# Kernel tuning notes

Measured on AMD Instinct MI355X. Metric: run time of the kernel, lower is better.

The kernel has to match this reference:

```python
import jax, jax.numpy as jnp
import numpy as np

N, E, R, B, IN, H, OUT, P = 20000, 320000, 8, 8, 128, 256, 128, 100000
LN_EPS = 1e-5


def _xavier(key, shape):
    fan_in, fan_out = shape[-2], shape[-1]
    lim = float(np.sqrt(6.0 / (fan_in + fan_out)))
    return jax.random.uniform(key, shape, jnp.float32, -lim, lim)


def setup_inputs() -> dict:
    key = jax.random.key(0)
    ks = iter(jax.random.split(key, 64))
    inp = {}
    inp['x'] = jax.random.normal(next(ks), (N, IN), jnp.float32)
    inp['edge_index'] = jax.random.randint(next(ks), (2, E), 0, N, jnp.int32)
    inp['edge_type'] = jax.random.randint(next(ks), (E,), 0, R, jnp.int32)
    inp['gene_pairs'] = jax.random.randint(next(ks), (2, P), 0, N, jnp.int32)
    dims = [(IN, H), (H, H), (H, H), (H, OUT)]  # per-layer (in_ch, out_ch)
    for i, (ic, oc) in enumerate(dims):
        inp[f'basis{i}'] = _xavier(next(ks), (B, ic, oc))
        inp[f'att{i}'] = _xavier(next(ks), (R, B))
        inp[f'root{i}'] = _xavier(next(ks), (ic, oc))
        inp[f'relatt{i}'] = jnp.ones((R,), jnp.float32)
        inp[f'g{i}'] = jnp.ones((oc,), jnp.float32)
        inp[f'b{i}'] = jnp.zeros((oc,), jnp.float32)
    inp['res0'] = _xavier(next(ks), (IN, H))   # in_ch != out_ch at layer 0
    inp['res3'] = _xavier(next(ks), (H, OUT))  # and at layer 3
    # decoder: 3*OUT -> H -> H//2 -> H//4 -> 1
    ddims = [(3 * OUT, H), (H, H // 2), (H // 2, H // 4), (H // 4, 1)]
    for i, (ic, oc) in enumerate(ddims):
        inp[f'dW{i}'] = _xavier(next(ks), (ic, oc))
        inp[f'db{i}'] = jnp.zeros((oc,), jnp.float32)
        if i < 3:
            inp[f'dg{i}'] = jnp.ones((oc,), jnp.float32)
            inp[f'dbb{i}'] = jnp.zeros((oc,), jnp.float32)
    return inp


def _ln(h, g, b):
    m = h.mean(-1, keepdims=True)
    v = ((h - m) ** 2).mean(-1, keepdims=True)
    return (h - m) * jax.lax.rsqrt(v + LN_EPS) * g + b


def _conv(x, src, dst, et, basis, att, root_w, rel_att):
    # W_r = sum_b att[r,b] * B_b ; message = a_{r(e)} * x_src @ W_{r(e)}
    # Since the message is linear, aggregate x_src per (dst, relation) first
    # (segment_sum), then apply the R small GEMMs once - same math, no [E,in,out].
    n, d = x.shape
    weight = jnp.einsum('rb,bio->rio', att, basis)          # [R,in,out]
    a = jax.nn.softmax(rel_att)                              # [R]
    seg = dst.astype(jnp.int32) * R + et.astype(jnp.int32)   # [(node,rel)] segment ids
    agg = jax.ops.segment_sum(x[src], seg, num_segments=n * R).reshape(n, R, d)
    out = jnp.einsum('nri,rio->no', agg, weight * a[:, None, None])
    return out + x @ root_w


def reference(x, edge_index, edge_type, gene_pairs,
              basis0, att0, root0, relatt0, g0, b0, res0,
              basis1, att1, root1, relatt1, g1, b1,
              basis2, att2, root2, relatt2, g2, b2,
              basis3, att3, root3, relatt3, g3, b3, res3,
              dW0, db0, dg0, dbb0, dW1, db1, dg1, dbb1,
              dW2, db2, dg2, dbb2, dW3, db3):
    src, dst = edge_index[0], edge_index[1]
    layers = [
        (basis0, att0, root0, relatt0, g0, b0, res0),
        (basis1, att1, root1, relatt1, g1, b1, None),
        (basis2, att2, root2, relatt2, g2, b2, None),
        (basis3, att3, root3, relatt3, g3, b3, res3),
    ]
    h = x
    for i, (bs, at, rt, ra, g, b, res) in enumerate(layers):
        h_in = h
        h = _conv(h, src, dst, edge_type, bs, at, rt, ra)
        h = _ln(h, g, b)
        h = h + (h_in @ res if res is not None else h_in)
        if i < len(layers) - 1:
            h = jax.nn.gelu(h, approximate=False)
    z = h  # [N, OUT]
    zi, zj = z[gene_pairs[0]], z[gene_pairs[1]]
    pe = jnp.concatenate([zi + zj, zi * zj, jnp.abs(zi - zj)], axis=-1)
    d = jax.nn.gelu(_ln(pe @ dW0 + db0, dg0, dbb0), approximate=False)
    d = jax.nn.gelu(_ln(d @ dW1 + db1, dg1, dbb1), approximate=False)
    d = jax.nn.gelu(_ln(d @ dW2 + db2, dg2, dbb2), approximate=False)
    logits = (d @ dW3 + db3).squeeze(-1)  # [P]
    return logits, z
```

## Files before the change

kernel.cpp:

```cpp
#include <hip/hip_runtime.h>
#include <hip/hip_bf16.h>
#include <math.h>
#include <cstddef>
#include <stdint.h>

#define NN 20000
#define EE 320000
#define RR 8
#define PP 100000
#define NR (NN * RR)

typedef __hip_bfloat16 bf16;
typedef __attribute__((ext_vector_type(8))) short short8;
typedef __attribute__((ext_vector_type(4))) short short4v;
typedef __attribute__((ext_vector_type(4))) float floatx4;
typedef __attribute__((ext_vector_type(4))) int intx4;

__device__ __forceinline__ float b2f(bf16 v) { return __bfloat162float(v); }
__device__ __forceinline__ bf16 f2b(float v) { return __float2bfloat16(v); }
__device__ __forceinline__ float bits2f(unsigned short u) {
  unsigned int i = ((unsigned int)u) << 16; float f; __builtin_memcpy(&f, &i, 4); return f;
}
__device__ __forceinline__ short f2bits(float f) {
  bf16 h = __float2bfloat16(f); short s; __builtin_memcpy(&s, &h, 2); return s;
}
__device__ __forceinline__ float gelu_f(float x) {
  float t = x * (0.7978845608f + 0.0356774081f * x * x);
  float s = exp2f(-2.885390082f * t);
  return x * __builtin_amdgcn_rcpf(1.f + s);
}
__device__ __forceinline__ void async_copy16(void* lds, const void* g) {
  __builtin_amdgcn_global_load_lds((const __attribute__((address_space(1))) void*)g,
                                   (__attribute__((address_space(3))) void*)lds, 16, 0, 0);
}
__device__ __forceinline__ const short8* frag_at(const bf16* base, int row, int q) {
  return (const short8*)(base + row * 64 + (((q) ^ (row & 7)) << 3));
}
__device__ __forceinline__ const short8* frag256(const bf16* base, int row, int col64, int q) {
  return (const short8*)(base + row * 256 + col64 + (((q) ^ (row & 7)) << 3));
}
__device__ __forceinline__ int idx128(int row, int qg) {
  return row * 128 + ((qg >> 3) << 6) + (((qg & 7) ^ (row & 7)) << 3);
}

__global__ void hist_k(const int* __restrict__ dst, const int* __restrict__ et,
                       int* __restrict__ counts) {
  int e = blockIdx.x * 256 + threadIdx.x;
  if (e >= EE) return;
  atomicAdd(&counts[dst[e] * RR + et[e]], 1);
}

__global__ void scan1_k(const int* __restrict__ counts, int* __restrict__ prefix,
                        int* __restrict__ bsums) {
  __shared__ int tmp[256];
  int i = blockIdx.x * 256 + threadIdx.x;
  int v = counts[i];
  tmp[threadIdx.x] = v; __syncthreads();
  for (int off = 1; off < 256; off <<= 1) {
    int x = (threadIdx.x >= off) ? tmp[threadIdx.x - off] : 0;
    __syncthreads();
    tmp[threadIdx.x] += x;
    __syncthreads();
  }
  prefix[i] = tmp[threadIdx.x] - v;
  if (threadIdx.x == 255) bsums[blockIdx.x] = tmp[255];
}

__global__ void scan2_k(int* __restrict__ bsums, int nb) {
  __shared__ int tmp[256];
  __shared__ int carry;
  if (threadIdx.x == 0) carry = 0;
  __syncthreads();
  for (int base = 0; base < nb; base += 256) {
    int i = base + threadIdx.x;
    int v = (i < nb) ? bsums[i] : 0;
    tmp[threadIdx.x] = v; __syncthreads();
    for (int off = 1; off < 256; off <<= 1) {
      int x = (threadIdx.x >= off) ? tmp[threadIdx.x - off] : 0;
      __syncthreads();
      tmp[threadIdx.x] += x;
      __syncthreads();
    }
    int c = carry;
    if (i < nb) bsums[i] = c + tmp[threadIdx.x] - v;
    __syncthreads();
    if (threadIdx.x == 255) carry = c + tmp[255];
    __syncthreads();
  }
}

__global__ void scan3_k(int* __restrict__ prefix, const int* __restrict__ bsums) {
  int i = blockIdx.x * 256 + threadIdx.x;
  prefix[i] += bsums[blockIdx.x];
}

__global__ void scatter_k(const int* __restrict__ src, const int* __restrict__ dst,
                          const int* __restrict__ et, const int* __restrict__ segstart,
                          int* __restrict__ cursor, int* __restrict__ ssrc) {
  int e = blockIdx.x * 256 + threadIdx.x;
  if (e >= EE) return;
  int s = dst[e] * RR + et[e];
  int pos = atomicAdd(&cursor[s], 1);
  ssrc[segstart[s] + pos] = src[e];
}

__global__ void cvt_bf16_k(const float* __restrict__ in, bf16* __restrict__ out, int n) {
  int i = blockIdx.x * 256 + threadIdx.x;
  if (i < n) out[i] = f2b(in[i]);
}

__global__ void softmax4_k(const float* r0, const float* r1, const float* r2,
                           const float* r3, float* __restrict__ a) {
  if (threadIdx.x == 0) {
    const float* rs[4] = {r0, r1, r2, r3};
    for (int l = 0; l < 4; ++l) {
      float mx = -1e30f;
      for (int i = 0; i < RR; ++i) mx = fmaxf(mx, rs[l][i]);
      float e[RR]; float s = 0.f;
      for (int i = 0; i < RR; ++i) { e[i] = expf(rs[l][i] - mx); s += e[i]; }
      for (int i = 0; i < RR; ++i) a[l * RR + i] = e[i] / s;
    }
  }
}

__global__ void transpose_k(const float* __restrict__ in, bf16* __restrict__ out,
                            int rows, int cols) {
  int idx = blockIdx.x * 256 + threadIdx.x;
  if (idx >= rows * cols) return;
  int r = idx / cols, c = idx - r * cols;
  out[(size_t)c * rows + r] = f2b(in[idx]);
}

__global__ void transpose_pe_k(const float* __restrict__ wb, const float* __restrict__ wc,
                               bf16* __restrict__ wpe) {
  int idx = blockIdx.x * 256 + threadIdx.x;
  if (idx >= 128 * 256) return;
  int k = idx >> 8;
  int o = idx & 255;
  wpe[(size_t)o * 256 + k] = f2b(wb[idx]);
  wpe[(size_t)o * 256 + 128 + k] = f2b(wc[idx]);
}

__global__ void prep_w_k(const float* __restrict__ basis, const float* __restrict__ att,
                         const float* __restrict__ root, const float* __restrict__ a,
                         bf16* __restrict__ Wt, int ic, int icsh, int oc, int ocsh) {
  int idx = blockIdx.x * 256 + threadIdx.x;
  int cols = 9 * ic;
  if (idx >= cols * oc) return;
  int o = idx & (oc - 1);
  int col = idx >> ocsh;
  int r = col >> icsh;
  int k = col & (ic - 1);
  float val;
  if (r < RR) {
    float acc = 0.f;
    for (int bb = 0; bb < RR; ++bb)
      acc += att[r * RR + bb] * basis[((size_t)bb * ic + k) * oc + o];
    val = a[r] * acc;
  } else {
    val = root[(size_t)k * oc + o];
  }
  Wt[(size_t)o * cols + col] = f2b(val);
}

__global__ __launch_bounds__(256) void aggregate_k(
    const bf16* __restrict__ h, const int* __restrict__ segstart,
    const int* __restrict__ counts, const int* __restrict__ ssrc,
    bf16* __restrict__ agg, int ic, int tpnsh) {
  int tpn = 1 << tpnsh;
  int npb = 256 >> tpnsh;
  int local = threadIdx.x >> tpnsh;
  int n = blockIdx.x * npb + local;
  if (n >= NN) return;
  int cbase = (threadIdx.x & (tpn - 1)) * 8;
  size_t rowoff = (size_t)n * (9 * ic);
  const bf16* hc = h + cbase;

  intx4 stv0 = *(const intx4*)(segstart + n * RR);
  intx4 stv1 = *(const intx4*)(segstart + n * RR + 4);
  intx4 ctv0 = *(const intx4*)(counts + n * RR);
  intx4 ctv1 = *(const intx4*)(counts + n * RR + 4);
  int sts[8] = {stv0[0], stv0[1], stv0[2], stv0[3], stv1[0], stv1[1], stv1[2], stv1[3]};
  int cts[8] = {ctv0[0], ctv0[1], ctv0[2], ctv0[3], ctv1[0], ctv1[1], ctv1[2], ctv1[3]};

#pragma unroll
  for (int rp = 0; rp < 4; ++rp) {
    const int stA = sts[rp],     cA = cts[rp];
    const int stB = sts[rp + 4], cB = cts[rp + 4];
    float aA[8] = {0.f, 0.f, 0.f, 0.f, 0.f, 0.f, 0.f, 0.f};
    float aB[8] = {0.f, 0.f, 0.f, 0.f, 0.f, 0.f, 0.f, 0.f};
    int iA = 0, iB = 0;
    while (iA + 2 <= cA && iB + 2 <= cB) {
      int sA0 = ssrc[stA + iA], sA1 = ssrc[stA + iA + 1];
      int sB0 = ssrc[stB + iB], sB1 = ssrc[stB + iB + 1];
      short8 vA0 = *(const short8*)(hc + (size_t)sA0 * ic);
      short8 vA1 = *(const short8*)(hc + (size_t)sA1 * ic);
      short8 vB0 = *(const short8*)(hc + (size_t)sB0 * ic);
      short8 vB1 = *(const short8*)(hc + (size_t)sB1 * ic);
#pragma unroll
      for (int j = 0; j < 8; ++j) {
        aA[j] += bits2f((unsigned short)vA0[j]) + bits2f((unsigned short)vA1[j]);
        aB[j] += bits2f((unsigned short)vB0[j]) + bits2f((unsigned short)vB1[j]);
      }
      iA += 2; iB += 2;
    }
    for (; iA + 2 <= cA; iA += 2) {
      int s0 = ssrc[stA + iA], s1 = ssrc[stA + iA + 1];
      short8 v0 = *(const short8*)(hc + (size_t)s0 * ic);
      short8 v1 = *(const short8*)(hc + (size_t)s1 * ic);
#pragma unroll
      for (int j = 0; j < 8; ++j)
        aA[j] += bits2f((unsigned short)v0[j]) + bits2f((unsigned short)v1[j]);
    }
    if (iA < cA) {
      int s0 = ssrc[stA + iA];
      short8 v0 = *(const short8*)(hc + (size_t)s0 * ic);
#pragma unroll
      for (int j = 0; j < 8; ++j) aA[j] += bits2f((unsigned short)v0[j]);
    }
    for (; iB + 2 <= cB; iB += 2) {
      int s0 = ssrc[stB + iB], s1 = ssrc[stB + iB + 1];
      short8 v0 = *(const short8*)(hc + (size_t)s0 * ic);
      short8 v1 = *(const short8*)(hc + (size_t)s1 * ic);
#pragma unroll
      for (int j = 0; j < 8; ++j)
        aB[j] += bits2f((unsigned short)v0[j]) + bits2f((unsigned short)v1[j]);
    }
    if (iB < cB) {
      int s0 = ssrc[stB + iB];
      short8 v0 = *(const short8*)(hc + (size_t)s0 * ic);
#pragma unroll
      for (int j = 0; j < 8; ++j) aB[j] += bits2f((unsigned short)v0[j]);
    }
    short8 oA, oB;
#pragma unroll
    for (int j = 0; j < 8; ++j) { oA[j] = f2bits(aA[j]); oB[j] = f2bits(aB[j]); }
    *(short8*)(agg + rowoff + rp * ic + cbase) = oA;
    *(short8*)(agg + rowoff + (rp + 4) * ic + cbase) = oB;
  }
  *(short8*)(agg + rowoff + 8 * ic + cbase) =
      *(const short8*)(h + (size_t)n * ic + cbase);
}

__global__ __launch_bounds__(256) void gemm_f32_k(
    const bf16* __restrict__ A, const bf16* __restrict__ Wt,
    float* __restrict__ Cf, int M, int N, int K, int nb) {
  const int bid = blockIdx.x;
  const int xcd = bid & 7;
  const int slot = bid >> 3;
  const int gidx = slot / nb;
  const int member = slot - gidx * nb;
  const int mb = (M + 127) >> 7;
  const int m = gidx * 8 + xcd;
  if (m >= mb) return;
  const int m0 = m * 128;
  const int n0 = member * 64;

  __shared__ __align__(16) bf16 As[128 * 128];
  __shared__ __align__(16) bf16 Ws[64 * 128];
  const int tid = threadIdx.x;
  const int wave = tid >> 6, lane = tid & 63;
  const int quad = lane >> 4, l16 = lane & 15;
  const int wm = (wave >> 1) * 64, wn = (wave & 1) * 32;
  floatx4 acc[4][2];
#pragma unroll
  for (int i = 0; i < 4; ++i)
#pragma unroll
    for (int j = 0; j < 2; ++j) acc[i][j] = (floatx4){0.f, 0.f, 0.f, 0.f};

  for (int k0 = 0; k0 < K; k0 += 128) {
#pragma unroll
    for (int q = 0; q < 8; ++q) {
      int c0 = (wave * 8 + q) * 1024;
      int r = (c0 >> 8) + (lane >> 4);
      int grow = m0 + r; if (grow >= M) grow = M - 1;
      int s = lane & 15;
      int qg = ((s >> 3) << 3) | ((s & 7) ^ (r & 7));
      async_copy16((char*)As + c0, A + (size_t)grow * K + k0 + qg * 8);
    }
#pragma unroll
    for (int q = 0; q < 4; ++q) {
      int c0 = (wave * 4 + q) * 1024;
      int r = (c0 >> 8) + (lane >> 4);
      int s = lane & 15;
      int qg = ((s >> 3) << 3) | ((s & 7) ^ (r & 7));
      async_copy16((char*)Ws + c0, Wt + (size_t)(n0 + r) * K + k0 + qg * 8);
    }
    __syncthreads();
#pragma unroll
    for (int kk = 0; kk < 4; ++kk) {
      int qg = kk * 4 + quad;
      short8 b0 = *(const short8*)(Ws + idx128(wn + l16, qg));
      short8 b1 = *(const short8*)(Ws + idx128(wn + 16 + l16, qg));
#pragma unroll
      for (int i = 0; i < 4; ++i) {
        short8 a = *(const short8*)(As + idx128(wm + i * 16 + l16, qg));
        acc[i][0] = __builtin_amdgcn_mfma_f32_16x16x32_bf16(a, b0, acc[i][0], 0, 0, 0);
        acc[i][1] = __builtin_amdgcn_mfma_f32_16x16x32_bf16(a, b1, acc[i][1], 0, 0, 0);
      }
    }
    __syncthreads();
  }
#pragma unroll
  for (int i = 0; i < 4; ++i)
#pragma unroll
    for (int j = 0; j < 2; ++j)
#pragma unroll
      for (int r = 0; r < 4; ++r) {
        int row = m0 + wm + i * 16 + quad * 4 + r;
        int col = n0 + wn + j * 16 + l16;
        if (row < M) Cf[(size_t)row * N + col] = acc[i][j][r];
      }
}

__global__ __launch_bounds__(256) void gemm_plain_k(
    const bf16* __restrict__ A, const bf16* __restrict__ Wt,
    bf16* __restrict__ Cb, int M, int N, int K) {
  __shared__ __align__(16) bf16 As[64 * 64];
  __shared__ __align__(16) bf16 Ws[64 * 64];
  const int m0 = blockIdx.y * 64;
  const int n0 = blockIdx.x * 64;
  const int tid = threadIdx.x;
  const int wave = tid >> 6, lane = tid & 63;
  const int quad = lane >> 4, l16 = lane & 15;
  const int wm = (wave >> 1) * 32, wn = (wave & 1) * 32;
  floatx4 acc00 = {0.f, 0.f, 0.f, 0.f};
  floatx4 acc01 = acc00, acc10 = acc00, acc11 = acc00;

  for (int k0 = 0; k0 < K; k0 += 64) {
#pragma unroll
    for (int q = 0; q < 2; ++q) {
      int c0 = (wave * 2 + q) * 1024;
      int row = (c0 >> 7) + (lane >> 3);
      int grow = m0 + row; if (grow >= M) grow = M - 1;
      int ch = (lane & 7) ^ (row & 7);
      async_copy16((char*)As + c0, A + (size_t)grow * K + k0 + ch * 8);
    }
#pragma unroll
    for (int q = 0; q < 2; ++q) {
      int c0 = (wave * 2 + q) * 1024;
      int row = (c0 >> 7) + (lane >> 3);
      int ch = (lane & 7) ^ (row & 7);
      async_copy16((char*)Ws + c0, Wt + (size_t)(n0 + row) * K + k0 + ch * 8);
    }
    __syncthreads();
#pragma unroll
    for (int kk = 0; kk < 64; kk += 32) {
      int qb = (kk >> 3) + quad;
      short8 a0 = *frag_at(As, wm + l16, qb);
      short8 a1 = *frag_at(As, wm + 16 + l16, qb);
      short8 b0 = *frag_at(Ws, wn + l16, qb);
      short8 b1 = *frag_at(Ws, wn + 16 + l16, qb);
      acc00 = __builtin_amdgcn_mfma_f32_16x16x32_bf16(a0, b0, acc00, 0, 0, 0);
      acc01 = __builtin_amdgcn_mfma_f32_16x16x32_bf16(a0, b1, acc01, 0, 0, 0);
      acc10 = __builtin_amdgcn_mfma_f32_16x16x32_bf16(a1, b0, acc10, 0, 0, 0);
      acc11 = __builtin_amdgcn_mfma_f32_16x16x32_bf16(a1, b1, acc11, 0, 0, 0);
    }
    __syncthreads();
  }
  floatx4 accs[2][2] = {{acc00, acc01}, {acc10, acc11}};
#pragma unroll
  for (int i = 0; i < 2; ++i)
#pragma unroll
    for (int j = 0; j < 2; ++j)
#pragma unroll
      for (int r = 0; r < 4; ++r) {
        int row = m0 + wm + i * 16 + quad * 4 + r;
        int col = n0 + wn + j * 16 + l16;
        if (row < M) Cb[(size_t)row * N + col] = f2b(accs[i][j][r]);
      }
}

__global__ __launch_bounds__(256) void ln_conv_k(
    const float* __restrict__ conv, const bf16* __restrict__ res,
    const float* __restrict__ g, const float* __restrict__ b,
    bf16* __restrict__ out, float* __restrict__ zout, int oc, int do_gelu) {
  int wave = threadIdx.x >> 6, lane = threadIdx.x & 63;
  int row = blockIdx.x * 4 + wave;
  if (row >= NN) return;
  int ne = oc >> 6;
  float v[4];
  float s = 0.f, s2 = 0.f;
  for (int i = 0; i < ne; ++i) {
    v[i] = conv[(size_t)row * oc + i * 64 + lane];
    s += v[i]; s2 += v[i] * v[i];
  }
  for (int off = 32; off; off >>= 1) { s += __shfl_xor(s, off); s2 += __shfl_xor(s2, off); }
  float m = s / oc;
  float var = s2 / oc - m * m;
  float rs = rsqrtf(var + 1e-5f);
  for (int i = 0; i < ne; ++i) {
    int c = i * 64 + lane;
    float y = (v[i] - m) * rs * g[c] + b[c];
    y += b2f(res[(size_t)row * oc + c]);
    if (zout) zout[(size_t)row * oc + c] = y;
    if (do_gelu) y = gelu_f(y);
    out[(size_t)row * oc + c] = f2b(y);
  }
}

__global__ __launch_bounds__(256) void gemm_pe_k(
    const bf16* __restrict__ z, const int* __restrict__ pairs,
    const bf16* __restrict__ WPE,
    bf16* __restrict__ P0) {
  const int bid = blockIdx.x;
  const int xcd = bid & 7;
  const int slot = bid >> 3;
  const int gidx = slot >> 1;
  const int member = slot & 1;
  const int mb = (PP + 127) >> 7;
  const int m = gidx * 8 + xcd;
  if (m >= mb) return;
  const int m0 = m * 128;
  const int n0 = member * 128;

  __shared__ __align__(16) bf16 PEs[128 * 128];
  __shared__ __align__(16) bf16 Ws[128 * 128];
  const int tid = threadIdx.x;
  const int wave = tid >> 6, lane = tid & 63;
  const int quad = lane >> 4, l16 = lane & 15;
  const int wm = (wave >> 1) * 64, wn = (wave & 1) * 64;

  const int prow = tid >> 1;
  const int h = tid & 1;
  int pp = m0 + prow; if (pp >= PP) pp = PP - 1;
  const bf16* zi = z + (size_t)pairs[pp] * 128;
  const bf16* zj = z + (size_t)pairs[PP + pp] * 128;

  floatx4 acc[4][4];
#pragma unroll
  for (int i = 0; i < 4; ++i)
#pragma unroll
    for (int j = 0; j < 4; ++j) acc[i][j] = (floatx4){0.f, 0.f, 0.f, 0.f};

#pragma unroll
  for (int kwi = 0; kwi < 2; ++kwi) {
    const int kw = kwi * 64;
    short8 va[4], vb[4];
#pragma unroll
    for (int c8 = 0; c8 < 4; ++c8) {
      va[c8] = *(const short8*)(zi + kw + h * 32 + c8 * 8);
      vb[c8] = *(const short8*)(zj + kw + h * 32 + c8 * 8);
    }
    if (kwi) __syncthreads();
#pragma unroll
    for (int q = 0; q < 8; ++q) {
      int c0 = (wave * 8 + q) * 1024;
      int r = (c0 >> 8) + (lane >> 4);
      int s = lane & 15;
      async_copy16((char*)Ws + c0,
                   WPE + (size_t)(n0 + r) * 256 + ((s >> 3) << 7) + kw + (((s & 7) ^ (r & 7)) << 3));
    }
#pragma unroll
    for (int c8 = 0; c8 < 4; ++c8) {
      short8 op, od;
#pragma unroll
      for (int jj = 0; jj < 8; ++jj) {
        float fa = bits2f((unsigned short)va[c8][jj]);
        float fb = bits2f((unsigned short)vb[c8][jj]);
        op[jj] = f2bits(fa * fb);
        od[jj] = f2bits(fabsf(fa - fb));
      }
      *(short8*)(PEs + idx128(prow, h * 4 + c8)) = op;
      *(short8*)(PEs + idx128(prow, 8 + h * 4 + c8)) = od;
    }
    __syncthreads();
#pragma unroll
    for (int ks = 0; ks < 4; ++ks) {
      const int qg = ks * 4 + quad;
      short8 bfr[4];
#pragma unroll
      for (int j = 0; j < 4; ++j)
        bfr[j] = *(const short8*)(Ws + idx128(wn + j * 16 + l16, qg));
#pragma unroll
      for (int i = 0; i < 4; ++i) {
        short8 a = *(const short8*)(PEs + idx128(wm + i * 16 + l16, qg));
#pragma unroll
        for (int j = 0; j < 4; ++j)
          acc[i][j] = __builtin_amdgcn_mfma_f32_16x16x32_bf16(a, bfr[j], acc[i][j], 0, 0, 0);
      }
    }
  }

#pragma unroll
  for (int i = 0; i < 4; ++i)
#pragma unroll
    for (int j = 0; j < 4; ++j)
#pragma unroll
      for (int r = 0; r < 4; ++r) {
        int row = m0 + wm + i * 16 + quad * 4 + r;
        int col = n0 + wn + j * 16 + l16;
        if (row < PP) P0[(size_t)row * 256 + col] = f2b(acc[i][j][r]);
      }
}

__global__ __launch_bounds__(256) void ln_d0_k(bf16* __restrict__ D0,
                                               const int* __restrict__ pairs,
                                               const bf16* __restrict__ ZA,
                                               const float* __restrict__ db0,
                                               const float* __restrict__ g,
                                               const float* __restrict__ b) {
  const int wave = threadIdx.x >> 6, lane = threadIdx.x & 63;
  const int row = blockIdx.x * 8 + wave * 2 + (lane >> 5);
  const int cb = (lane & 31) * 8;
  int gi = pairs[row], gj = pairs[PP + row];
  bf16* p = D0 + (size_t)row * 256 + cb;
  short8 xv = *(const short8*)p;
  short8 av = *(const short8*)(ZA + (size_t)gi * 256 + cb);
  short8 bv = *(const short8*)(ZA + (size_t)gj * 256 + cb);
  float v[8];
  float s = 0.f, s2 = 0.f;
#pragma unroll
  for (int k = 0; k < 8; ++k) {
    v[k] = bits2f((unsigned short)xv[k]) + bits2f((unsigned short)av[k]) +
           bits2f((unsigned short)bv[k]) + db0[cb + k];
    s += v[k]; s2 += v[k] * v[k];
  }
  for (int off = 16; off; off >>= 1) { s += __shfl_xor(s, off); s2 += __shfl_xor(s2, off); }
  float m = s / 256.f;
  float var = s2 / 256.f - m * m;
  float rs = rsqrtf(var + 1e-5f);
  short8 ov;
#pragma unroll
  for (int k = 0; k < 8; ++k) {
    float y = (v[k] - m) * rs * g[cb + k] + b[cb + k];
    ov[k] = f2bits(gelu_f(y));
  }
  *(short8*)p = ov;
}

__global__ __launch_bounds__(256) void lngemm1_k(
    const bf16* __restrict__ D0, const bf16* __restrict__ W1t,
    const float* __restrict__ bias, bf16* __restrict__ P1, int M) {
  __shared__ __align__(16) bf16 As[64 * 256];
  __shared__ __align__(16) bf16 Ws[128 * 64];
  const int tid = threadIdx.x;
  const int wave = tid >> 6, lane = tid & 63;
  const int quad = lane >> 4, l16 = lane & 15;
  const int wr = (wave >> 1) * 32;
  const int wc = (wave & 1) * 64;
  const int m0 = blockIdx.x * 64;

  {
    const int srow = tid >> 2;
    const int q4 = tid & 3;
    int grow = m0 + srow; if (grow >= M) grow = M - 1;
    const bf16* src = D0 + (size_t)grow * 256 + q4 * 64;
#pragma unroll
    for (int c8 = 0; c8 < 8; ++c8) {
      short8 o = *(const short8*)(src + c8 * 8);
      *(short8*)(As + srow * 256 + q4 * 64 + ((c8 ^ (srow & 7)) << 3)) = o;
    }
  }

  floatx4 acc[2][4];
#pragma unroll
  for (int i = 0; i < 2; ++i)
#pragma unroll
    for (int j = 0; j < 4; ++j) acc[i][j] = (floatx4){0.f, 0.f, 0.f, 0.f};

  for (int kc = 0; kc < 4; ++kc) {
#pragma unroll
    for (int q = 0; q < 4; ++q) {
      int c0 = q * 4096 + wave * 1024;
      int row = (c0 >> 7) + (lane >> 3);
      int ch = (lane & 7) ^ (row & 7);
      async_copy16((char*)Ws + c0, W1t + (size_t)row * 256 + kc * 64 + ch * 8);
    }
    __syncthreads();
#pragma unroll
    for (int kk = 0; kk < 64; kk += 32) {
      int qb = (kk >> 3) + quad;
      short8 a0 = *frag256(As, wr + l16, kc * 64, qb);
      short8 a1 = *frag256(As, wr + 16 + l16, kc * 64, qb);
#pragma unroll
      for (int j = 0; j < 4; ++j) {
        short8 bb = *frag_at(Ws, wc + j * 16 + l16, qb);
        acc[0][j] = __builtin_amdgcn_mfma_f32_16x16x32_bf16(a0, bb, acc[0][j], 0, 0, 0);
        acc[1][j] = __builtin_amdgcn_mfma_f32_16x16x32_bf16(a1, bb, acc[1][j], 0, 0, 0);
      }
    }
    __syncthreads();
  }

#pragma unroll
  for (int i = 0; i < 2; ++i)
#pragma unroll
    for (int r = 0; r < 4; ++r) {
      int row = wr + i * 16 + quad * 4 + r;
      int grow = m0 + row;
      if (grow >= M) continue;
#pragma unroll
      for (int j = 0; j < 4; ++j) {
        int col = wc + j * 16 + l16;
        P1[(size_t)grow * 128 + col] = f2b(acc[i][j][r] + bias[col]);
      }
    }
}

__global__ __launch_bounds__(256) void lngemm2_k(
    const bf16* __restrict__ P1, const bf16* __restrict__ W2t,
    const float* __restrict__ g, const float* __restrict__ b,
    const float* __restrict__ bias, bf16* __restrict__ P2, int M) {
  __shared__ __align__(16) bf16 As[64 * 128];
  __shared__ __align__(16) bf16 Ws[64 * 64];
  const int tid = threadIdx.x;
  const int wave = tid >> 6, lane = tid & 63;
  const int quad = lane >> 4, l16 = lane & 15;
  const int m0 = blockIdx.x * 64;

  {
    const int srow = tid >> 2;
    const int q4 = tid & 3;
    int grow = m0 + srow; if (grow >= M) grow = M - 1;
    const bf16* src = P1 + (size_t)grow * 128 + q4 * 32;
    float v[32];
    float s = 0.f, s2 = 0.f;
#pragma unroll
    for (int c8 = 0; c8 < 4; ++c8) {
      short8 x = *(const short8*)(src + c8 * 8);
#pragma unroll
      for (int jj = 0; jj < 8; ++jj) {
        float f = bits2f((unsigned short)x[jj]);
        v[c8 * 8 + jj] = f; s += f; s2 += f * f;
      }
    }
    s += __shfl_xor(s, 1); s2 += __shfl_xor(s2, 1);
    s += __shfl_xor(s, 2); s2 += __shfl_xor(s2, 2);
    float mean = s / 128.f;
    float var = s2 / 128.f - mean * mean;
    float rs = rsqrtf(var + 1e-5f);
#pragma unroll
    for (int c8 = 0; c8 < 4; ++c8) {
      short8 o;
#pragma unroll
      for (int jj = 0; jj < 8; ++jj) {
        int col = q4 * 32 + c8 * 8 + jj;
        float y = (v[c8 * 8 + jj] - mean) * rs * g[col] + b[col];
        o[jj] = f2bits(gelu_f(y));
      }
      *(short8*)(As + idx128(srow, q4 * 4 + c8)) = o;
    }
  }

  floatx4 acc[4];
#pragma unroll
  for (int j = 0; j < 4; ++j) acc[j] = (floatx4){0.f, 0.f, 0.f, 0.f};

  for (int kc = 0; kc < 2; ++kc) {
#pragma unroll
    for (int q = 0; q < 2; ++q) {
      int c0 = q * 4096 + wave * 1024;
      int row = (c0 >> 7) + (lane >> 3);
      int ch = (lane & 7) ^ (row & 7);
      async_copy16((char*)Ws + c0, W2t + (size_t)row * 128 + kc * 64 + ch * 8);
    }
    __syncthreads();
#pragma unroll
    for (int kk = 0; kk < 64; kk += 32) {
      int qb = (kk >> 3) + quad;
      short8 a = *(const short8*)(As + idx128(wave * 16 + l16, kc * 8 + qb));
#pragma unroll
      for (int j = 0; j < 4; ++j) {
        short8 bb = *frag_at(Ws, j * 16 + l16, qb);
        acc[j] = __builtin_amdgcn_mfma_f32_16x16x32_bf16(a, bb, acc[j], 0, 0, 0);
      }
    }
    __syncthreads();
  }

#pragma unroll
  for (int r = 0; r < 4; ++r) {
    int row = wave * 16 + quad * 4 + r;
    int grow = m0 + row;
    if (grow >= M) continue;
#pragma unroll
    for (int j = 0; j < 4; ++j) {
      int col = j * 16 + l16;
      P2[(size_t)grow * 64 + col] = f2b(acc[j][r] + bias[col]);
    }
  }
}

__global__ __launch_bounds__(256) void logits_k(const bf16* __restrict__ P2,
                                                const float* __restrict__ g,
                                                const float* __restrict__ b,
                                                const float* __restrict__ w3,
                                                const float* __restrict__ b3,
                                                float* __restrict__ out) {
  int wave = threadIdx.x >> 6, lane = threadIdx.x & 63;
  int p = blockIdx.x * 4 + wave;
  if (p >= PP) return;
  float v = b2f(P2[(size_t)p * 64 + lane]);
  float s = v, s2 = v * v;
  for (int off = 32; off; off >>= 1) { s += __shfl_xor(s, off); s2 += __shfl_xor(s2, off); }
  float m = s / 64.f;
  float var = s2 / 64.f - m * m;
  float rs = rsqrtf(var + 1e-5f);
  float y = gelu_f((v - m) * rs * g[lane] + b[lane]);
  float t = y * w3[lane];
  for (int off = 32; off; off >>= 1) t += __shfl_xor(t, off);
  if (lane == 0) out[p] = t + b3[0];
}

extern "C" void kernel_launch(void* const* d_in, const int* in_sizes, int n_in,
                              void* d_out, int out_size, void* d_ws, size_t ws_size,
                              hipStream_t stream) {
  auto cdiv = [](int a, int b) { return (a + b - 1) / b; };

  const float* x = (const float*)d_in[0];
  const int* ei = (const int*)d_in[1];
  const int* et = (const int*)d_in[2];
  const int* gp = (const int*)d_in[3];
  const float *basis[4], *att[4], *root[4], *relatt[4], *gln[4], *bln[4];
  for (int l = 0; l < 4; ++l) {
    basis[l]  = (const float*)d_in[4 + 6 * l];
    att[l]    = (const float*)d_in[5 + 6 * l];
    root[l]   = (const float*)d_in[6 + 6 * l];
    relatt[l] = (const float*)d_in[7 + 6 * l];
    gln[l]    = (const float*)d_in[8 + 6 * l];
    bln[l]    = (const float*)d_in[9 + 6 * l];
  }
  const float* res0 = (const float*)d_in[28];
  const float* res3 = (const float*)d_in[29];
  const float* dW0 = (const float*)d_in[30]; const float* db0 = (const float*)d_in[31];
  const float* dg0 = (const float*)d_in[32]; const float* dbb0 = (const float*)d_in[33];
  const float* dW1 = (const float*)d_in[34]; const float* db1 = (const float*)d_in[35];
  const float* dg1 = (const float*)d_in[36]; const float* dbb1 = (const float*)d_in[37];
  const float* dW2 = (const float*)d_in[38]; const float* db2 = (const float*)d_in[39];
  const float* dg2 = (const float*)d_in[40]; const float* dbb2 = (const float*)d_in[41];
  const float* dW3 = (const float*)d_in[42]; const float* db3 = (const float*)d_in[43];

  char* base = (char*)d_ws;
  size_t off = 0;
  auto alloc = [&](size_t bytes) -> char* {
    char* p = base + off;
    off += (bytes + 255) & ~(size_t)255;
    return p;
  };
  bf16* X16 = (bf16*)alloc((size_t)NN * 128 * 2);
  bf16* HA  = (bf16*)alloc((size_t)NN * 256 * 2);
  bf16* HB  = (bf16*)alloc((size_t)NN * 256 * 2);
  bf16* RESB = (bf16*)alloc((size_t)NN * 256 * 2);
  bf16* ZA   = (bf16*)alloc((size_t)NN * 256 * 2);
  float* CONV = (float*)alloc((size_t)NN * 256 * 4);
  bf16* WT    = (bf16*)alloc((size_t)589824 * 2);
  bf16* RES0T = (bf16*)alloc((size_t)32768 * 2);
  bf16* RES3T = (bf16*)alloc((size_t)32768 * 2);
  bf16* WAT   = (bf16*)alloc((size_t)32768 * 2);
  bf16* WPE   = (bf16*)alloc((size_t)65536 * 2);
  bf16* DW1T  = (bf16*)alloc((size_t)32768 * 2);
  bf16* DW2T  = (bf16*)alloc((size_t)8192 * 2);
  float* ASOFT = (float*)alloc(32 * 4);
  int* COUNTS = (int*)alloc((size_t)NR * 4);
  int* SEG    = (int*)alloc((size_t)NR * 4);
  int* CUR    = (int*)alloc((size_t)NR * 4);
  int* BS     = (int*)alloc(1024 * 4);
  int* SSRC   = (int*)alloc((size_t)EE * 4);
  char* BIG = alloc(93000000);
  bf16* AGG = (bf16*)BIG;
  bf16* P0  = (bf16*)BIG;
  bf16* P1  = (bf16*)alloc((size_t)PP * 128 * 2);
  bf16* P2  = (bf16*)alloc((size_t)PP * 64 * 2);
  (void)ws_size; (void)in_sizes; (void)n_in; (void)out_size;

  float* out_logits = (float*)d_out;
  float* out_z = (float*)d_out + PP;

  hipMemsetAsync(COUNTS, 0, (size_t)NR * 4, stream);
  hipMemsetAsync(CUR, 0, (size_t)NR * 4, stream);
  hist_k<<<cdiv(EE, 256), 256, 0, stream>>>(ei + EE, et, COUNTS);
  scan1_k<<<NR / 256, 256, 0, stream>>>(COUNTS, SEG, BS);
  scan2_k<<<1, 256, 0, stream>>>(BS, NR / 256);
  scan3_k<<<NR / 256, 256, 0, stream>>>(SEG, BS);
  scatter_k<<<cdiv(EE, 256), 256, 0, stream>>>(ei, ei + EE, et, SEG, CUR, SSRC);

  cvt_bf16_k<<<cdiv(NN * 128, 256), 256, 0, stream>>>(x, X16, NN * 128);
  softmax4_k<<<1, 64, 0, stream>>>(relatt[0], relatt[1], relatt[2], relatt[3], ASOFT);
  transpose_k<<<cdiv(128 * 256, 256), 256, 0, stream>>>(res0, RES0T, 128, 256);
  transpose_k<<<cdiv(256 * 128, 256), 256, 0, stream>>>(res3, RES3T, 256, 128);
  transpose_k<<<cdiv(128 * 256, 256), 256, 0, stream>>>(dW0, WAT, 128, 256);
  transpose_pe_k<<<cdiv(128 * 256, 256), 256, 0, stream>>>(dW0 + 128 * 256, dW0 + 256 * 256, WPE);
  transpose_k<<<cdiv(256 * 128, 256), 256, 0, stream>>>(dW1, DW1T, 256, 128);
  transpose_k<<<cdiv(128 * 64, 256), 256, 0, stream>>>(dW2, DW2T, 128, 64);

  const int mb = cdiv(NN, 128);
  const int swzP4 = 8 * cdiv(mb, 8) * 4;
  const int swzP2 = 8 * cdiv(mb, 8) * 2;

  prep_w_k<<<cdiv(9 * 128 * 256, 256), 256, 0, stream>>>(basis[0], att[0], root[0], ASOFT + 0, WT, 128, 7, 256, 8);
  aggregate_k<<<cdiv(NN, 16), 256, 0, stream>>>(X16, SEG, COUNTS, SSRC, AGG, 128, 4);
  gemm_plain_k<<<dim3(4, cdiv(NN, 64)), 256, 0, stream>>>(X16, RES0T, RESB, NN, 256, 128);
  gemm_f32_k<<<swzP4, 256, 0, stream>>>(AGG, WT, CONV, NN, 256, 1152, 4);
  ln_conv_k<<<cdiv(NN, 4), 256, 0, stream>>>(CONV, RESB, gln[0], bln[0], HA, nullptr, 256, 1);

  prep_w_k<<<cdiv(9 * 256 * 256, 256), 256, 0, stream>>>(basis[1], att[1], root[1], ASOFT + 8, WT, 256, 8, 256, 8);
  aggregate_k<<<cdiv(NN, 8), 256, 0, stream>>>(HA, SEG, COUNTS, SSRC, AGG, 256, 5);
  gemm_f32_k<<<swzP4, 256, 0, stream>>>(AGG, WT, CONV, NN, 256, 2304, 4);
  ln_conv_k<<<cdiv(NN, 4), 256, 0, stream>>>(CONV, HA, gln[1], bln[1], HB, nullptr, 256, 1);

  prep_w_k<<<cdiv(9 * 256 * 256, 256), 256, 0, stream>>>(basis[2], att[2], root[2], ASOFT + 16, WT, 256, 8, 256, 8);
  aggregate_k<<<cdiv(NN, 8), 256, 0, stream>>>(HB, SEG, COUNTS, SSRC, AGG, 256, 5);
  gemm_f32_k<<<swzP4, 256, 0, stream>>>(AGG, WT, CONV, NN, 256, 2304, 4);
  ln_conv_k<<<cdiv(NN, 4), 256, 0, stream>>>(CONV, HB, gln[2], bln[2], HA, nullptr, 256, 1);

  prep_w_k<<<cdiv(9 * 256 * 128, 256), 256, 0, stream>>>(basis[3], att[3], root[3], ASOFT + 24, WT, 256, 8, 128, 7);
  aggregate_k<<<cdiv(NN, 8), 256, 0, stream>>>(HA, SEG, COUNTS, SSRC, AGG, 256, 5);
  gemm_plain_k<<<dim3(2, cdiv(NN, 64)), 256, 0, stream>>>(HA, RES3T, RESB, NN, 128, 256);
  gemm_f32_k<<<swzP2, 256, 0, stream>>>(AGG, WT, CONV, NN, 128, 2304, 2);
  ln_conv_k<<<cdiv(NN, 4), 256, 0, stream>>>(CONV, RESB, gln[3], bln[3], HB, out_z, 128, 0);

  gemm_plain_k<<<dim3(4, cdiv(NN, 64)), 256, 0, stream>>>(HB, WAT, ZA, NN, 256, 128);
  const int pb = cdiv(PP, 128);
  const int swzPE = 8 * cdiv(pb, 8) * 2;
  gemm_pe_k<<<swzPE, 256, 0, stream>>>(HB, gp, WPE, P0);
  ln_d0_k<<<cdiv(PP, 8), 256, 0, stream>>>(P0, gp, ZA, db0, dg0, dbb0);
  lngemm1_k<<<cdiv(PP, 64), 256, 0, stream>>>(P0, DW1T, db1, P1, PP);
  lngemm2_k<<<cdiv(PP, 64), 256, 0, stream>>>(P1, DW2T, dg1, dbb1, db2, P2, PP);
  logits_k<<<cdiv(PP, 4), 256, 0, stream>>>(P2, dg2, dbb2, dW3, db3, out_logits);
}
```

Measured before the change: 691.8 us.

## Fuse small transposes, store conv output as bf16, fuse logits into lngemm2

Six weight transpose launches are merged into one prep kernel. The conv GEMM now writes bf16 instead of fp32, and the LayerNorm kernel reads it with vectorized 8-wide loads, using fewer lanes per row. The final LayerNorm, GELU and dot-product logits step is folded into the lngemm2 epilogue, which removes the P2 buffer and one launch. The aim is to cut launch overhead and memory traffic, at the cost of extra bf16 rounding on the conv output before LayerNorm.

```diff
diff --git a/kernel.cpp b/kernel.cpp
--- a/kernel.cpp
+++ b/kernel.cpp
@@ -123,22 +123,33 @@
   }
 }
 
-__global__ void transpose_k(const float* __restrict__ in, bf16* __restrict__ out,
-                            int rows, int cols) {
+__global__ void prep_small_k(const float* __restrict__ res0, const float* __restrict__ res3,
+                             const float* __restrict__ dW0, const float* __restrict__ dW1,
+                             const float* __restrict__ dW2,
+                             bf16* __restrict__ RES0T, bf16* __restrict__ RES3T,
+                             bf16* __restrict__ WAT, bf16* __restrict__ WPE,
+                             bf16* __restrict__ DW1T, bf16* __restrict__ DW2T) {
   int idx = blockIdx.x * 256 + threadIdx.x;
-  if (idx >= rows * cols) return;
-  int r = idx / cols, c = idx - r * cols;
-  out[(size_t)c * rows + r] = f2b(in[idx]);
-}
-
-__global__ void transpose_pe_k(const float* __restrict__ wb, const float* __restrict__ wc,
-                               bf16* __restrict__ wpe) {
-  int idx = blockIdx.x * 256 + threadIdx.x;
-  if (idx >= 128 * 256) return;
-  int k = idx >> 8;
-  int o = idx & 255;
-  wpe[(size_t)o * 256 + k] = f2b(wb[idx]);
-  wpe[(size_t)o * 256 + 128 + k] = f2b(wc[idx]);
+  if (idx < 32768) {
+    int r = idx >> 8, c = idx & 255;
+    RES0T[(size_t)c * 128 + r] = f2b(res0[idx]);
+  } else if (idx < 65536) {
+    int i2 = idx - 32768; int r = i2 >> 7, c = i2 & 127;
+    RES3T[(size_t)c * 256 + r] = f2b(res3[i2]);
+  } else if (idx < 98304) {
+    int i2 = idx - 65536; int r = i2 >> 8, c = i2 & 255;
+    WAT[(size_t)c * 128 + r] = f2b(dW0[i2]);
+  } else if (idx < 131072) {
+    int i2 = idx - 98304; int k = i2 >> 8, o = i2 & 255;
+    WPE[(size_t)o * 256 + k] = f2b(dW0[128 * 256 + i2]);
+    WPE[(size_t)o * 256 + 128 + k] = f2b(dW0[256 * 256 + i2]);
+  } else if (idx < 163840) {
+    int i2 = idx - 131072; int r = i2 >> 7, c = i2 & 127;
+    DW1T[(size_t)c * 256 + r] = f2b(dW1[i2]);
+  } else if (idx < 172032) {
+    int i2 = idx - 163840; int r = i2 >> 6, c = i2 & 63;
+    DW2T[(size_t)c * 128 + r] = f2b(dW2[i2]);
+  }
 }
 
 __global__ void prep_w_k(const float* __restrict__ basis, const float* __restrict__ att,
@@ -244,7 +255,7 @@
 
 __global__ __launch_bounds__(256) void gemm_f32_k(
     const bf16* __restrict__ A, const bf16* __restrict__ Wt,
-    float* __restrict__ Cf, int M, int N, int K, int nb) {
+    bf16* __restrict__ Cb, int M, int N, int K, int nb) {
   const int bid = blockIdx.x;
   const int xcd = bid & 7;
   const int slot = bid >> 3;
@@ -309,7 +320,7 @@
       for (int r = 0; r < 4; ++r) {
         int row = m0 + wm + i * 16 + quad * 4 + r;
         int col = n0 + wn + j * 16 + l16;
-        if (row < M) Cf[(size_t)row * N + col] = acc[i][j][r];
+        if (row < M) Cb[(size_t)row * N + col] = f2b(acc[i][j][r]);
       }
 }
 
@@ -372,31 +383,39 @@
 }
 
 __global__ __launch_bounds__(256) void ln_conv_k(
-    const float* __restrict__ conv, const bf16* __restrict__ res,
+    const bf16* __restrict__ conv, const bf16* __restrict__ res,
     const float* __restrict__ g, const float* __restrict__ b,
     bf16* __restrict__ out, float* __restrict__ zout, int oc, int do_gelu) {
-  int wave = threadIdx.x >> 6, lane = threadIdx.x & 63;
-  int row = blockIdx.x * 4 + wave;
+  const int lprsh = (oc == 256) ? 5 : 4;
+  const int lpr = 1 << lprsh;
+  const int rpb = 256 >> lprsh;
+  int row = blockIdx.x * rpb + (threadIdx.x >> lprsh);
   if (row >= NN) return;
-  int ne = oc >> 6;
-  float v[4];
+  int cb = (threadIdx.x & (lpr - 1)) * 8;
+  short8 cv = *(const short8*)(conv + (size_t)row * oc + cb);
+  float v[8];
   float s = 0.f, s2 = 0.f;
-  for (int i = 0; i < ne; ++i) {
-    v[i] = conv[(size_t)row * oc + i * 64 + lane];
-    s += v[i]; s2 += v[i] * v[i];
-  }
-  for (int off = 32; off; off >>= 1) { s += __shfl_xor(s, off); s2 += __shfl_xor(s2, off); }
+#pragma unroll
+  for (int j = 0; j < 8; ++j) {
+    v[j] = bits2f((unsigned short)cv[j]);
+    s += v[j]; s2 += v[j] * v[j];
+  }
+  for (int off = lpr >> 1; off; off >>= 1) { s += __shfl_xor(s, off); s2 += __shfl_xor(s2, off); }
   float m = s / oc;
   float var = s2 / oc - m * m;
   float rs = rsqrtf(var + 1e-5f);
-  for (int i = 0; i < ne; ++i) {
-    int c = i * 64 + lane;
-    float y = (v[i] - m) * rs * g[c] + b[c];
-    y += b2f(res[(size_t)row * oc + c]);
+  short8 rv = *(const short8*)(res + (size_t)row * oc + cb);
+  short8 ov;
+#pragma unroll
+  for (int j = 0; j < 8; ++j) {
+    int c = cb + j;
+    float y = (v[j] - m) * rs * g[c] + b[c];
+    y += bits2f((unsigned short)rv[j]);
     if (zout) zout[(size_t)row * oc + c] = y;
     if (do_gelu) y = gelu_f(y);
-    out[(size_t)row * oc + c] = f2b(y);
-  }
+    ov[j] = f2bits(y);
+  }
+  *(short8*)(out + (size_t)row * oc + cb) = ov;
 }
 
 __global__ __launch_bounds__(256) void gemm_pe_k(
@@ -601,7 +620,10 @@
 __global__ __launch_bounds__(256) void lngemm2_k(
     const bf16* __restrict__ P1, const bf16* __restrict__ W2t,
     const float* __restrict__ g, const float* __restrict__ b,
-    const float* __restrict__ bias, bf16* __restrict__ P2, int M) {
+    const float* __restrict__ bias,
+    const float* __restrict__ g2, const float* __restrict__ b2,
+    const float* __restrict__ w3, const float* __restrict__ b3,
+    float* __restrict__ out, int M) {
   __shared__ __align__(16) bf16 As[64 * 128];
   __shared__ __align__(16) bf16 Ws[64 * 64];
   const int tid = threadIdx.x;
@@ -673,34 +695,28 @@
   for (int r = 0; r < 4; ++r) {
     int row = wave * 16 + quad * 4 + r;
     int grow = m0 + row;
-    if (grow >= M) continue;
+    float y[4];
+    float s = 0.f, s2 = 0.f;
 #pragma unroll
     for (int j = 0; j < 4; ++j) {
       int col = j * 16 + l16;
-      P2[(size_t)grow * 64 + col] = f2b(acc[j][r] + bias[col]);
-    }
-  }
-}
-
-__global__ __launch_bounds__(256) void logits_k(const bf16* __restrict__ P2,
-                                                const float* __restrict__ g,
-                                                const float* __restrict__ b,
-                                                const float* __restrict__ w3,
-                                                const float* __restrict__ b3,
-                                                float* __restrict__ out) {
-  int wave = threadIdx.x >> 6, lane = threadIdx.x & 63;
-  int p = blockIdx.x * 4 + wave;
-  if (p >= PP) return;
-  float v = b2f(P2[(size_t)p * 64 + lane]);
-  float s = v, s2 = v * v;
-  for (int off = 32; off; off >>= 1) { s += __shfl_xor(s, off); s2 += __shfl_xor(s2, off); }
-  float m = s / 64.f;
-  float var = s2 / 64.f - m * m;
-  float rs = rsqrtf(var + 1e-5f);
-  float y = gelu_f((v - m) * rs * g[lane] + b[lane]);
-  float t = y * w3[lane];
-  for (int off = 32; off; off >>= 1) t += __shfl_xor(t, off);
-  if (lane == 0) out[p] = t + b3[0];
+      y[j] = acc[j][r] + bias[col];
+      s += y[j]; s2 += y[j] * y[j];
+    }
+    for (int off = 8; off; off >>= 1) { s += __shfl_xor(s, off); s2 += __shfl_xor(s2, off); }
+    float mean = s / 64.f;
+    float var = s2 / 64.f - mean * mean;
+    float rs = rsqrtf(var + 1e-5f);
+    float t = 0.f;
+#pragma unroll
+    for (int j = 0; j < 4; ++j) {
+      int col = j * 16 + l16;
+      float yy = gelu_f((y[j] - mean) * rs * g2[col] + b2[col]);
+      t += yy * w3[col];
+    }
+    for (int off = 8; off; off >>= 1) t += __shfl_xor(t, off);
+    if (l16 == 0 && grow < M) out[grow] = t + b3[0];
+  }
 }
 
 extern "C" void kernel_launch(void* const* d_in, const int* in_sizes, int n_in,
@@ -743,7 +759,7 @@
   bf16* HB  = (bf16*)alloc((size_t)NN * 256 * 2);
   bf16* RESB = (bf16*)alloc((size_t)NN * 256 * 2);
   bf16* ZA   = (bf16*)alloc((size_t)NN * 256 * 2);
-  float* CONV = (float*)alloc((size_t)NN * 256 * 4);
+  bf16* CONV = (bf16*)alloc((size_t)NN * 256 * 2);
   bf16* WT    = (bf16*)alloc((size_t)589824 * 2);
   bf16* RES0T = (bf16*)alloc((size_t)32768 * 2);
   bf16* RES3T = (bf16*)alloc((size_t)32768 * 2);
@@ -761,7 +777,6 @@
   bf16* AGG = (bf16*)BIG;
   bf16* P0  = (bf16*)BIG;
   bf16* P1  = (bf16*)alloc((size_t)PP * 128 * 2);
-  bf16* P2  = (bf16*)alloc((size_t)PP * 64 * 2);
   (void)ws_size; (void)in_sizes; (void)n_in; (void)out_size;
 
   float* out_logits = (float*)d_out;
@@ -777,12 +792,8 @@
 
   cvt_bf16_k<<<cdiv(NN * 128, 256), 256, 0, stream>>>(x, X16, NN * 128);
   softmax4_k<<<1, 64, 0, stream>>>(relatt[0], relatt[1], relatt[2], relatt[3], ASOFT);
-  transpose_k<<<cdiv(128 * 256, 256), 256, 0, stream>>>(res0, RES0T, 128, 256);
-  transpose_k<<<cdiv(256 * 128, 256), 256, 0, stream>>>(res3, RES3T, 256, 128);
-  transpose_k<<<cdiv(128 * 256, 256), 256, 0, stream>>>(dW0, WAT, 128, 256);
-  transpose_pe_k<<<cdiv(128 * 256, 256), 256, 0, stream>>>(dW0 + 128 * 256, dW0 + 256 * 256, WPE);
-  transpose_k<<<cdiv(256 * 128, 256), 256, 0, stream>>>(dW1, DW1T, 256, 128);
-  transpose_k<<<cdiv(128 * 64, 256), 256, 0, stream>>>(dW2, DW2T, 128, 64);
+  prep_small_k<<<cdiv(172032, 256), 256, 0, stream>>>(res0, res3, dW0, dW1, dW2,
+                                                      RES0T, RES3T, WAT, WPE, DW1T, DW2T);
 
   const int mb = cdiv(NN, 128);
   const int swzP4 = 8 * cdiv(mb, 8) * 4;
@@ -792,23 +803,23 @@
   aggregate_k<<<cdiv(NN, 16), 256, 0, stream>>>(X16, SEG, COUNTS, SSRC, AGG, 128, 4);
   gemm_plain_k<<<dim3(4, cdiv(NN, 64)), 256, 0, stream>>>(X16, RES0T, RESB, NN, 256, 128);
   gemm_f32_k<<<swzP4, 256, 0, stream>>>(AGG, WT, CONV, NN, 256, 1152, 4);
-  ln_conv_k<<<cdiv(NN, 4), 256, 0, stream>>>(CONV, RESB, gln[0], bln[0], HA, nullptr, 256, 1);
+  ln_conv_k<<<cdiv(NN, 8), 256, 0, stream>>>(CONV, RESB, gln[0], bln[0], HA, nullptr, 256, 1);
 
   prep_w_k<<<cdiv(9 * 256 * 256, 256), 256, 0, stream>>>(basis[1], att[1], root[1], ASOFT + 8, WT, 256, 8, 256, 8);
   aggregate_k<<<cdiv(NN, 8), 256, 0, stream>>>(HA, SEG, COUNTS, SSRC, AGG, 256, 5);
   gemm_f32_k<<<swzP4, 256, 0, stream>>>(AGG, WT, CONV, NN, 256, 2304, 4);
-  ln_conv_k<<<cdiv(NN, 4), 256, 0, stream>>>(CONV, HA, gln[1], bln[1], HB, nullptr, 256, 1);
+  ln_conv_k<<<cdiv(NN, 8), 256, 0, stream>>>(CONV, HA, gln[1], bln[1], HB, nullptr, 256, 1);
 
   prep_w_k<<<cdiv(9 * 256 * 256, 256), 256, 0, stream>>>(basis[2], att[2], root[2], ASOFT + 16, WT, 256, 8, 256, 8);
   aggregate_k<<<cdiv(NN, 8), 256, 0, stream>>>(HB, SEG, COUNTS, SSRC, AGG, 256, 5);
   gemm_f32_k<<<swzP4, 256, 0, stream>>>(AGG, WT, CONV, NN, 256, 2304, 4);
-  ln_conv_k<<<cdiv(NN, 4), 256, 0, stream>>>(CONV, HB, gln[2], bln[2], HA, nullptr, 256, 1);
+  ln_conv_k<<<cdiv(NN, 8), 256, 0, stream>>>(CONV, HB, gln[2], bln[2], HA, nullptr, 256, 1);
 
   prep_w_k<<<cdiv(9 * 256 * 128, 256), 256, 0, stream>>>(basis[3], att[3], root[3], ASOFT + 24, WT, 256, 8, 128, 7);
   aggregate_k<<<cdiv(NN, 8), 256, 0, stream>>>(HA, SEG, COUNTS, SSRC, AGG, 256, 5);
   gemm_plain_k<<<dim3(2, cdiv(NN, 64)), 256, 0, stream>>>(HA, RES3T, RESB, NN, 128, 256);
   gemm_f32_k<<<swzP2, 256, 0, stream>>>(AGG, WT, CONV, NN, 128, 2304, 2);
-  ln_conv_k<<<cdiv(NN, 4), 256, 0, stream>>>(CONV, RESB, gln[3], bln[3], HB, out_z, 128, 0);
+  ln_conv_k<<<cdiv(NN, 16), 256, 0, stream>>>(CONV, RESB, gln[3], bln[3], HB, out_z, 128, 0);
 
   gemm_plain_k<<<dim3(4, cdiv(NN, 64)), 256, 0, stream>>>(HB, WAT, ZA, NN, 256, 128);
   const int pb = cdiv(PP, 128);
@@ -816,6 +827,6 @@
   gemm_pe_k<<<swzPE, 256, 0, stream>>>(HB, gp, WPE, P0);
   ln_d0_k<<<cdiv(PP, 8), 256, 0, stream>>>(P0, gp, ZA, db0, dg0, dbb0);
   lngemm1_k<<<cdiv(PP, 64), 256, 0, stream>>>(P0, DW1T, db1, P1, PP);
-  lngemm2_k<<<cdiv(PP, 64), 256, 0, stream>>>(P1, DW2T, dg1, dbb1, db2, P2, PP);
-  logits_k<<<cdiv(PP, 4), 256, 0, stream>>>(P2, dg2, dbb2, dW3, db3, out_logits);
-}
+  lngemm2_k<<<cdiv(PP, 64), 256, 0, stream>>>(P1, DW2T, dg1, dbb1, db2, dg2, dbb2,
+                                              dW3, db3, out_logits, PP);
+}
```

Result: no change. 696.0 us (+0.6%).
